# Kernel optimization log

Measured on AMD Instinct MI355X. Metric: run time of the kernel, lower is better.

The kernel has to match this reference:

```python
import jax, jax.numpy as jnp
import numpy as np

N, D_IN, D_OUT, E = 50000, 64, 64, 800000
NEG_SLOPE = 0.2  # PyG GATConv default leaky-relu slope


def setup_inputs() -> dict:
    key = jax.random.key(0)
    ks = jax.random.split(key, 11)
    s_in = 1.0 / np.sqrt(D_IN)
    s_out = 1.0 / np.sqrt(D_OUT)
    return {
        "x": jax.random.normal(ks[0], (N, D_IN), jnp.float32),
        "edge_index": jax.random.randint(ks[1], (2, E), 0, N, jnp.int32),
        "h": jax.random.normal(ks[2], (N, D_OUT), jnp.float32) * 0.1,
        "c": jax.random.normal(ks[3], (N, D_OUT), jnp.float32) * 0.1,
        "W": jax.random.normal(ks[4], (4, D_IN, D_OUT), jnp.float32) * s_in,
        "b": jax.random.normal(ks[5], (4, 1, D_OUT), jnp.float32) * 0.01,
        "Wsrc": jax.random.normal(ks[6], (4, D_OUT, D_OUT), jnp.float32) * s_out,
        "Wdst": jax.random.normal(ks[7], (4, D_OUT, D_OUT), jnp.float32) * s_out,
        "att_src": jax.random.normal(ks[8], (4, D_OUT), jnp.float32) * 0.1,
        "att_dst": jax.random.normal(ks[9], (4, D_OUT), jnp.float32) * 0.1,
        "gat_b": jax.random.normal(ks[10], (4, D_OUT), jnp.float32) * 0.01,
    }


def _gat(h, src, dst, Ws, Wd, a_s, a_d, bg, n):
    """GATConv(heads=1, add_self_loops=False) on edges src->dst."""
    hs = h @ Ws                      # [N, D] source-side projection
    hd = h @ Wd                      # [N, D] dest-side projection
    alpha_s = hs @ a_s               # [N]
    alpha_d = hd @ a_d               # [N]
    e = jax.nn.leaky_relu(alpha_s[src] + alpha_d[dst], NEG_SLOPE)  # [E]
    # numerically stable segment softmax over incoming edges per dst node
    m = jax.ops.segment_max(e, dst, num_segments=n)
    ex = jnp.exp(e - m[dst])
    denom = jax.ops.segment_sum(ex, dst, num_segments=n)
    w = ex / denom[dst]              # [E] attention weights
    out = jax.ops.segment_sum(w[:, None] * hs[src], dst, num_segments=n)
    return out + bg


def reference(x, edge_index, h, c, W, b, Wsrc, Wdst, att_src, att_dst, gat_b):
    src, dst = edge_index[0], edge_index[1]
    n = x.shape[0]

    def gate(g, act):
        pre = x @ W[g] + _gat(h, src, dst, Wsrc[g], Wdst[g],
                              att_src[g], att_dst[g], gat_b[g], n) + b[g]
        return act(pre)

    i = gate(0, jax.nn.sigmoid)
    f = gate(1, jax.nn.sigmoid)
    t = gate(2, jnp.tanh)
    c_new = f * c + i * t
    o = gate(3, jax.nn.sigmoid)   # output gate conv uses the OLD hidden state h
    h_new = o * jnp.tanh(c_new)
    return (h_new, c_new)
```

## Files before the change

### kernel.cpp

```cpp
#include <hip/hip_runtime.h>
#include <math.h>

#define NEG_SLOPE 0.2f

typedef float  f32x4 __attribute__((ext_vector_type(4)));
typedef short  s16x8 __attribute__((ext_vector_type(8)));

__device__ __forceinline__ unsigned short bfr(float a){
  unsigned u = __float_as_uint(a);
  return (unsigned short)((u + 0x7FFFu + ((u>>16)&1u)) >> 16);
}
__device__ __forceinline__ float bf2f(unsigned short s){
  return __uint_as_float(((unsigned)s)<<16);
}
__device__ __forceinline__ ushort4 packf4(float4 v){
  ushort4 r; r.x=bfr(v.x); r.y=bfr(v.y); r.z=bfr(v.z); r.w=bfr(v.w); return r;
}

__device__ __forceinline__ signed char q8(float v){
  int q = __float2int_rn(v * 128.f);
  q = q > 127 ? 127 : (q < -127 ? -127 : q);
  return (signed char)q;
}

__global__ void k_wvec_pack(const float* __restrict__ Wsrc, const float* __restrict__ Wdst,
                            const float* __restrict__ Wmain,
                            const float* __restrict__ att_src, const float* __restrict__ att_dst,
                            float* __restrict__ wvec, int* __restrict__ bcnt,
                            unsigned short* __restrict__ pw, unsigned short* __restrict__ ps){
  int tid = threadIdx.x;
  if (blockIdx.x == 0){
    if (tid < 128) bcnt[tid] = 0;
    int v = tid >> 6, t = tid & 63;
    const float* M = (v<4) ? (Wsrc + v*4096) : (Wdst + (v-4)*4096);
    const float* a = (v<4) ? (att_src + v*64) : (att_dst + (v-4)*64);
    float s = 0.f;
    for (int k=0;k<64;++k) s += M[t*64+k]*a[k];
    wvec[v*64+t] = s;
  } else {
    int vv = (blockIdx.x-1)*512 + tid;
    if (vv < 2048){
      int l = vv & 63, u = vv >> 6;
      int ct = u & 3, ks = (u>>2)&1, g = u>>3;
      int col = ct*16 + (l&15);
      int r0  = ks*32 + (l>>4)*8;
      #pragma unroll
      for (int j=0;j<8;++j){
        pw[vv*8+j] = bfr(Wmain[g*4096 + (r0+j)*64 + col]);
        ps[vv*8+j] = bfr(Wsrc [g*4096 + (r0+j)*64 + col]);
      }
    }
  }
}

__global__ __launch_bounds__(256) void k_pack(
    const float* __restrict__ x, const float* __restrict__ h,
    const float* __restrict__ wvec, const int* __restrict__ ei,
    unsigned short* __restrict__ xb, signed char* __restrict__ h8,
    float* __restrict__ alphas, int* __restrict__ bcnt, int shift, int N, int E){
  __shared__ float hl[32*65];
  __shared__ float wl[8*65];
  __shared__ int   cb[128];
  int tid = threadIdx.x;
  int nbase = blockIdx.x*32;
  int nlim = min(32, N-nbase);
  int cnt = nlim*16;
  if (tid < 128) cb[tid] = 0;
  {
    const float4* hsrc = (const float4*)(h + (size_t)nbase*64);
    const float4* xsrc = (const float4*)(x + (size_t)nbase*64);
    char4* hdst = (char4*)(h8 + (size_t)nbase*64);
    ushort4* xdst = (ushort4*)(xb + (size_t)nbase*64);
    for (int i=tid; i<cnt; i+=256){
      float4 v = hsrc[i];
      int n = i>>4, t4 = (i&15)*4;
      float* d = hl + n*65 + t4;
      d[0]=v.x; d[1]=v.y; d[2]=v.z; d[3]=v.w;
      hdst[i] = make_char4(q8(v.x), q8(v.y), q8(v.z), q8(v.w));
      xdst[i] = packf4(xsrc[i]);
    }
    for (int i=tid; i<512; i+=256) wl[(i>>6)*65 + (i&63)] = wvec[i];
  }
  __syncthreads();
  int v = tid & 7, n = tid >> 3;
  if (n < nlim){
    const float* hp = hl + n*65;
    const float* wp = wl + v*65;
    float s = 0.f;
    #pragma unroll
    for (int t=0;t<64;++t) s += hp[t]*wp[t];
    alphas[(size_t)(nbase+n)*8 + v] = s;
  }
  int Q = E >> 2;
  const int4* d4 = (const int4*)(ei + E);
  long gs = (long)gridDim.x*256;
  for (long q=(long)blockIdx.x*256+tid; q<Q; q+=gs){
    int4 d = d4[q];
    atomicAdd(&cb[d.x>>shift],1); atomicAdd(&cb[d.y>>shift],1);
    atomicAdd(&cb[d.z>>shift],1); atomicAdd(&cb[d.w>>shift],1);
  }
  int tail = E - (Q<<2);
  if (blockIdx.x == 0 && tid < tail) atomicAdd(&cb[ei[E+(Q<<2)+tid]>>shift],1);
  __syncthreads();
  if (tid < 128 && cb[tid]) atomicAdd(&bcnt[tid], cb[tid]);
}

__global__ void k_bscan(const int* __restrict__ bcnt, int* __restrict__ bbase,
                        int* __restrict__ bfill, int* __restrict__ rowptr,
                        int nbuck, int N, int E){
  __shared__ int s[128];
  int tid = threadIdx.x;
  int x = (tid<nbuck) ? bcnt[tid] : 0;
  s[tid] = x;
  __syncthreads();
  for (int off=1; off<128; off<<=1){
    int t = (tid>=off) ? s[tid-off] : 0;
    __syncthreads();
    s[tid] += t;
    __syncthreads();
  }
  if (tid<nbuck){ int e = s[tid]-x; bbase[tid]=e; bfill[tid]=e; }
  if (tid==0){ bbase[nbuck]=E; rowptr[N]=E; }
}

__global__ __launch_bounds__(256) void k_bin(
    const int* __restrict__ ei, int* __restrict__ bfill,
    int2* __restrict__ binned, int shift, int E){
  __shared__ int2 buf[2048];
  __shared__ int cnt[128], off[128], gbase[128];
  int tid = threadIdx.x;
  int c0 = blockIdx.x*2048;
  int m = min(2048, E - c0);
  if (m <= 0) return;
  for (int i=tid; i<128; i+=256) cnt[i] = 0;
  __syncthreads();
  int myb[8], myslot[8], mysrc[8], mydst[8];
  #pragma unroll
  for (int j=0;j<8;++j){
    int k = tid + j*256;
    if (k < m){
      int e = c0 + k;
      mysrc[j] = ei[e];
      mydst[j] = ei[E+e];
      int bkt = mydst[j] >> shift;
      myb[j] = bkt;
      myslot[j] = atomicAdd(&cnt[bkt], 1);
    } else myb[j] = -1;
  }
  __syncthreads();
  if (tid == 0){
    int acc = 0;
    for (int i=0;i<128;++i){ off[i] = acc; acc += cnt[i]; }
  }
  __syncthreads();
  #pragma unroll
  for (int j=0;j<8;++j)
    if (myb[j] >= 0) buf[off[myb[j]] + myslot[j]] = make_int2(mysrc[j], mydst[j]);
  if (tid < 128 && cnt[tid] > 0) gbase[tid] = atomicAdd(&bfill[tid], cnt[tid]);
  __syncthreads();
  for (int i=tid; i<m; i+=256){
    int2 p = buf[i];
    int bkt = p.y >> shift;
    binned[gbase[bkt] + (i - off[bkt])] = p;
  }
}

__global__ __launch_bounds__(1024) void k_place(
    const int2* __restrict__ binned, const int* __restrict__ bbase,
    int* __restrict__ rowptr, int* __restrict__ csr_src, int shift, int N){
  __shared__ int cnt[1024];
  __shared__ int tsum[1024];
  int tid = threadIdx.x;
  int d0 = blockIdx.x << shift;
  if (d0 >= N) return;
  int dpb = 1 << shift;
  int dlim = min(dpb, N - d0);
  if (tid < dpb) cnt[tid] = 0;
  __syncthreads();
  int base = bbase[blockIdx.x], end = bbase[blockIdx.x+1];
  for (int i = base + tid; i < end; i += 1024)
    atomicAdd(&cnt[binned[i].y - d0], 1);
  __syncthreads();
  int xv = (tid < dpb) ? cnt[tid] : 0;
  tsum[tid] = xv;
  __syncthreads();
  for (int off=1; off<1024; off<<=1){
    int t = (tid>=off) ? tsum[tid-off] : 0;
    __syncthreads();
    tsum[tid] += t;
    __syncthreads();
  }
  if (tid < dpb) cnt[tid] = tsum[tid] - xv + base;
  __syncthreads();
  if (tid < dlim) rowptr[d0+tid] = cnt[tid];
  __syncthreads();
  for (int i = base + tid; i < end; i += 1024){
    int2 p = binned[i];
    int pos = atomicAdd(&cnt[p.y - d0], 1);
    csr_src[pos] = p.x;
  }
}

__global__ __launch_bounds__(256) void k_agg(
    const int* __restrict__ csr_src, const int* __restrict__ rowptr,
    const float* __restrict__ alphas,
    const signed char* __restrict__ h8, unsigned short* __restrict__ aggb, int N){
  __shared__ float4 wb4[4][64];
  __shared__ int    sb[4][64];
  int wave = threadIdx.x>>6, lane = threadIdx.x&63;
  int dst = blockIdx.x*4 + wave;
  if (dst >= N) return;
  int base = rowptr[dst];
  int d = rowptr[dst+1] - base;
  float4 ad = ((const float4*)alphas)[(size_t)dst*2+1];
  float ss0=0.f,ss1=0.f,ss2=0.f,ss3=0.f;
  float a0=0.f,a1=0.f,a2=0.f,a3=0.f;
  for (int c0=0; c0<d; c0+=64){
    int cnt = min(64, d-c0);
    if (lane < cnt){
      int s = csr_src[base+c0+lane];
      float4 as = ((const float4*)alphas)[(size_t)s*2];
      float e0=as.x+ad.x; e0 = e0>0.f ? e0 : NEG_SLOPE*e0; float x0=__expf(e0); ss0+=x0;
      float e1=as.y+ad.y; e1 = e1>0.f ? e1 : NEG_SLOPE*e1; float x1=__expf(e1); ss1+=x1;
      float e2=as.z+ad.z; e2 = e2>0.f ? e2 : NEG_SLOPE*e2; float x2=__expf(e2); ss2+=x2;
      float e3=as.w+ad.w; e3 = e3>0.f ? e3 : NEG_SLOPE*e3; float x3=__expf(e3); ss3+=x3;
      sb[wave][lane] = s;
      wb4[wave][lane] = make_float4(x0,x1,x2,x3);
    }
    asm volatile("" ::: "memory");
    int j = 0;
    for (; j+3 < cnt; j += 4){
      int s0_ = sb[wave][j],   s1_ = sb[wave][j+1];
      int s2_ = sb[wave][j+2], s3_ = sb[wave][j+3];
      float4 w0_ = wb4[wave][j],   w1_ = wb4[wave][j+1];
      float4 w2_ = wb4[wave][j+2], w3_ = wb4[wave][j+3];
      float h0_ = (float)h8[(size_t)s0_*64 + lane];
      float h1_ = (float)h8[(size_t)s1_*64 + lane];
      float h2_ = (float)h8[(size_t)s2_*64 + lane];
      float h3_ = (float)h8[(size_t)s3_*64 + lane];
      a0 += w0_.x*h0_; a1 += w0_.y*h0_; a2 += w0_.z*h0_; a3 += w0_.w*h0_;
      a0 += w1_.x*h1_; a1 += w1_.y*h1_; a2 += w1_.z*h1_; a3 += w1_.w*h1_;
      a0 += w2_.x*h2_; a1 += w2_.y*h2_; a2 += w2_.z*h2_; a3 += w2_.w*h2_;
      a0 += w3_.x*h3_; a1 += w3_.y*h3_; a2 += w3_.z*h3_; a3 += w3_.w*h3_;
    }
    for (; j < cnt; ++j){
      int sj = sb[wave][j];
      float4 wj = wb4[wave][j];
      float hv = (float)h8[(size_t)sj*64 + lane];
      a0 += wj.x*hv; a1 += wj.y*hv; a2 += wj.z*hv; a3 += wj.w*hv;
    }
    asm volatile("" ::: "memory");
  }
  #pragma unroll
  for (int off=32; off; off>>=1){
    ss0 += __shfl_xor(ss0, off, 64);
    ss1 += __shfl_xor(ss1, off, 64);
    ss2 += __shfl_xor(ss2, off, 64);
    ss3 += __shfl_xor(ss3, off, 64);
  }
  size_t o = (size_t)dst*64 + lane;
  size_t NE = (size_t)N*64;
  if (d>0){
    aggb[o]      = bfr(a0/(ss0*128.f));
    aggb[NE+o]   = bfr(a1/(ss1*128.f));
    aggb[2*NE+o] = bfr(a2/(ss2*128.f));
    aggb[3*NE+o] = bfr(a3/(ss3*128.f));
  } else {
    aggb[o] = 0; aggb[NE+o] = 0; aggb[2*NE+o] = 0; aggb[3*NE+o] = 0;
  }
}

__global__ __launch_bounds__(256) void k_fused(
    const unsigned short* __restrict__ xb, const unsigned short* __restrict__ aggb,
    const unsigned short* __restrict__ pw, const unsigned short* __restrict__ ps,
    const float* __restrict__ b, const float* __restrict__ gat_b,
    const float* __restrict__ c, float* __restrict__ out, int N){
  __shared__ unsigned short Pl[4][32][68];
  int tid = threadIdx.x, g = tid>>6, l = tid&63;
  int lr = l & 15;
  int lq = l >> 4;
  int nbase = blockIdx.x*32;
  int nlim = min(32, N-nbase);

  s16x8 BW[2][4], BS[2][4];
  #pragma unroll
  for (int ks=0; ks<2; ++ks){
    #pragma unroll
    for (int ct=0; ct<4; ++ct){
      size_t idx = ((size_t)((g*2+ks)*4+ct)*64 + l)*8;
      BW[ks][ct] = *(const s16x8*)(pw + idx);
      BS[ks][ct] = *(const s16x8*)(ps + idx);
    }
  }

  s16x8 AX[2][2], AG[2][2];
  #pragma unroll
  for (int rt=0; rt<2; ++rt){
    int row = nbase + rt*16 + lr;
    if (row >= N) row = N-1;
    #pragma unroll
    for (int ks=0; ks<2; ++ks){
      AX[rt][ks] = *(const s16x8*)(xb   + (size_t)row*64 + ks*32 + lq*8);
      AG[rt][ks] = *(const s16x8*)(aggb + ((size_t)g*N + row)*64 + ks*32 + lq*8);
    }
  }

  #pragma unroll
  for (int rt=0; rt<2; ++rt){
    #pragma unroll
    for (int ct=0; ct<4; ++ct){
      int col = ct*16 + lr;
      float bias = b[g*64 + col] + gat_b[g*64 + col];
      f32x4 acc = {bias, bias, bias, bias};
      #pragma unroll
      for (int ks=0; ks<2; ++ks){
        acc = __builtin_amdgcn_mfma_f32_16x16x32_bf16(AX[rt][ks], BW[ks][ct], acc, 0,0,0);
        acc = __builtin_amdgcn_mfma_f32_16x16x32_bf16(AG[rt][ks], BS[ks][ct], acc, 0,0,0);
      }
      #pragma unroll
      for (int r=0;r<4;++r)
        Pl[g][rt*16 + lq*4 + r][col] = bfr(acc[r]);
    }
  }
  __syncthreads();

  size_t NE = (size_t)N*64;
  #pragma unroll
  for (int n=0; n<8; ++n){
    int node = g*8 + n;
    if (node < nlim){
      size_t o = (size_t)(nbase + node)*64 + l;
      float p0 = bf2f(Pl[0][node][l]);
      float p1 = bf2f(Pl[1][node][l]);
      float p2 = bf2f(Pl[2][node][l]);
      float p3 = bf2f(Pl[3][node][l]);
      float ig = 1.f/(1.f + __expf(-p0));
      float fg = 1.f/(1.f + __expf(-p1));
      float tg = tanhf(p2);
      float og = 1.f/(1.f + __expf(-p3));
      float cn = fg*c[o] + ig*tg;
      out[o]      = og*tanhf(cn);
      out[NE + o] = cn;
    }
  }
}

extern "C" void kernel_launch(void* const* d_in, const int* in_sizes, int n_in,
                              void* d_out, int out_size, void* d_ws, size_t ws_size,
                              hipStream_t stream){
  const float* x       = (const float*)d_in[0];
  const int*   ei      = (const int*)d_in[1];
  const float* h       = (const float*)d_in[2];
  const float* c       = (const float*)d_in[3];
  const float* W       = (const float*)d_in[4];
  const float* b       = (const float*)d_in[5];
  const float* Wsrc    = (const float*)d_in[6];
  const float* Wdst    = (const float*)d_in[7];
  const float* att_src = (const float*)d_in[8];
  const float* att_dst = (const float*)d_in[9];
  const float* gat_b   = (const float*)d_in[10];
  float* out = (float*)d_out;

  int N = in_sizes[0] / 64;
  int E = in_sizes[1] / 2;

  int shift = 9;
  while (((N + (1<<shift) - 1) >> shift) > 128) shift++;
  int nbuck = (N + (1<<shift) - 1) >> shift;

  unsigned short* aggb = (unsigned short*)d_ws;
  unsigned short* xb   = aggb + (size_t)4*N*64;
  signed char*    h8   = (signed char*)(xb + (size_t)N*64);
  unsigned short* pw   = (unsigned short*)(h8 + (size_t)N*64);
  unsigned short* ps   = pw   + 16384;
  float* alphas = (float*)(ps + 16384);
  int* csr_src  = (int*)(alphas + (size_t)N*8);
  int2* binned  = (int2*)(csr_src + ((E+3)&~3));
  int* rowptr   = (int*)(binned + E);
  int* bcnt     = rowptr + N + 1;
  int* bbase    = bcnt + 128;
  int* bfill    = bbase + 129;
  float* wvec   = (float*)(bfill + 128);

  k_wvec_pack<<<9, 512, 0, stream>>>(Wsrc, Wdst, W, att_src, att_dst, wvec, bcnt, pw, ps);
  k_pack  <<<(N+31)/32, 256, 0, stream>>>(x, h, wvec, ei, xb, h8, alphas, bcnt, shift, N, E);
  k_bscan <<<1, 128, 0, stream>>>(bcnt, bbase, bfill, rowptr, nbuck, N, E);
  k_bin   <<<(E + 2047)/2048, 256, 0, stream>>>(ei, bfill, binned, shift, E);
  k_place <<<nbuck, 1024, 0, stream>>>(binned, bbase, rowptr, csr_src, shift, N);
  k_agg   <<<(N+3)/4, 256, 0, stream>>>(csr_src, rowptr, alphas, h8, aggb, N);
  k_fused <<<(N+31)/32, 256, 0, stream>>>(xb, aggb, pw, ps, b, gat_b, c, out, N);
}
```

Baseline: 127.9 us.

## Precompute bf16 source attention scores during binning and store in CSR order

Source-side attention logits are gathered in the binning kernel, rounded to bf16, and carried through the binned records into a new CSR-ordered weight array. The aggregation kernel then reads these scores contiguously instead of gathering 16-byte alpha rows per edge by source index. The cost is wider binned records, an extra per-edge array write and read, a random gather moved into k_bin, and reduced precision of alpha_s.

```diff
diff --git a/kernel.cpp b/kernel.cpp
--- a/kernel.cpp
+++ b/kernel.cpp
@@ -124,9 +124,9 @@
 }
 
 __global__ __launch_bounds__(256) void k_bin(
-    const int* __restrict__ ei, int* __restrict__ bfill,
-    int2* __restrict__ binned, int shift, int E){
-  __shared__ int2 buf[2048];
+    const int* __restrict__ ei, const float* __restrict__ alphas,
+    int* __restrict__ bfill, int4* __restrict__ binned, int shift, int E){
+  __shared__ int4 buf[2048];
   __shared__ int cnt[128], off[128], gbase[128];
   int tid = threadIdx.x;
   int c0 = blockIdx.x*2048;
@@ -135,13 +135,18 @@
   for (int i=tid; i<128; i+=256) cnt[i] = 0;
   __syncthreads();
   int myb[8], myslot[8], mysrc[8], mydst[8];
+  int myw0[8], myw1[8];
   #pragma unroll
   for (int j=0;j<8;++j){
     int k = tid + j*256;
     if (k < m){
       int e = c0 + k;
-      mysrc[j] = ei[e];
+      int s = ei[e];
+      mysrc[j] = s;
       mydst[j] = ei[E+e];
+      float4 as = ((const float4*)alphas)[(size_t)s*2];
+      myw0[j] = (int)(((unsigned)bfr(as.x)) | (((unsigned)bfr(as.y))<<16));
+      myw1[j] = (int)(((unsigned)bfr(as.z)) | (((unsigned)bfr(as.w))<<16));
       int bkt = mydst[j] >> shift;
       myb[j] = bkt;
       myslot[j] = atomicAdd(&cnt[bkt], 1);
@@ -155,19 +160,20 @@
   __syncthreads();
   #pragma unroll
   for (int j=0;j<8;++j)
-    if (myb[j] >= 0) buf[off[myb[j]] + myslot[j]] = make_int2(mysrc[j], mydst[j]);
+    if (myb[j] >= 0) buf[off[myb[j]] + myslot[j]] = make_int4(mysrc[j], mydst[j], myw0[j], myw1[j]);
   if (tid < 128 && cnt[tid] > 0) gbase[tid] = atomicAdd(&bfill[tid], cnt[tid]);
   __syncthreads();
   for (int i=tid; i<m; i+=256){
-    int2 p = buf[i];
+    int4 p = buf[i];
     int bkt = p.y >> shift;
     binned[gbase[bkt] + (i - off[bkt])] = p;
   }
 }
 
 __global__ __launch_bounds__(1024) void k_place(
-    const int2* __restrict__ binned, const int* __restrict__ bbase,
-    int* __restrict__ rowptr, int* __restrict__ csr_src, int shift, int N){
+    const int4* __restrict__ binned, const int* __restrict__ bbase,
+    int* __restrict__ rowptr, int* __restrict__ csr_src, int2* __restrict__ csr_w,
+    int shift, int N){
   __shared__ int cnt[1024];
   __shared__ int tsum[1024];
   int tid = threadIdx.x;
@@ -195,15 +201,16 @@
   if (tid < dlim) rowptr[d0+tid] = cnt[tid];
   __syncthreads();
   for (int i = base + tid; i < end; i += 1024){
-    int2 p = binned[i];
+    int4 p = binned[i];
     int pos = atomicAdd(&cnt[p.y - d0], 1);
     csr_src[pos] = p.x;
+    csr_w[pos] = make_int2(p.z, p.w);
   }
 }
 
 __global__ __launch_bounds__(256) void k_agg(
-    const int* __restrict__ csr_src, const int* __restrict__ rowptr,
-    const float* __restrict__ alphas,
+    const int* __restrict__ csr_src, const int2* __restrict__ csr_w,
+    const int* __restrict__ rowptr, const float* __restrict__ alphas,
     const signed char* __restrict__ h8, unsigned short* __restrict__ aggb, int N){
   __shared__ float4 wb4[4][64];
   __shared__ int    sb[4][64];
@@ -219,11 +226,11 @@
     int cnt = min(64, d-c0);
     if (lane < cnt){
       int s = csr_src[base+c0+lane];
-      float4 as = ((const float4*)alphas)[(size_t)s*2];
-      float e0=as.x+ad.x; e0 = e0>0.f ? e0 : NEG_SLOPE*e0; float x0=__expf(e0); ss0+=x0;
-      float e1=as.y+ad.y; e1 = e1>0.f ? e1 : NEG_SLOPE*e1; float x1=__expf(e1); ss1+=x1;
-      float e2=as.z+ad.z; e2 = e2>0.f ? e2 : NEG_SLOPE*e2; float x2=__expf(e2); ss2+=x2;
-      float e3=as.w+ad.w; e3 = e3>0.f ? e3 : NEG_SLOPE*e3; float x3=__expf(e3); ss3+=x3;
+      int2 wp = csr_w[base+c0+lane];
+      float e0 = bf2f((unsigned short)(wp.x & 0xFFFF)) + ad.x; e0 = e0>0.f ? e0 : NEG_SLOPE*e0; float x0=__expf(e0); ss0+=x0;
+      float e1 = bf2f((unsigned short)((unsigned)wp.x >> 16)) + ad.y; e1 = e1>0.f ? e1 : NEG_SLOPE*e1; float x1=__expf(e1); ss1+=x1;
+      float e2 = bf2f((unsigned short)(wp.y & 0xFFFF)) + ad.z; e2 = e2>0.f ? e2 : NEG_SLOPE*e2; float x2=__expf(e2); ss2+=x2;
+      float e3 = bf2f((unsigned short)((unsigned)wp.y >> 16)) + ad.w; e3 = e3>0.f ? e3 : NEG_SLOPE*e3; float x3=__expf(e3); ss3+=x3;
       sb[wave][lane] = s;
       wb4[wave][lane] = make_float4(x0,x1,x2,x3);
     }
@@ -375,8 +382,9 @@
   unsigned short* ps   = pw   + 16384;
   float* alphas = (float*)(ps + 16384);
   int* csr_src  = (int*)(alphas + (size_t)N*8);
-  int2* binned  = (int2*)(csr_src + ((E+3)&~3));
-  int* rowptr   = (int*)(binned + E);
+  int4* binned  = (int4*)(csr_src + ((E+3)&~3));
+  int2* csr_w   = (int2*)(binned + E);
+  int* rowptr   = (int*)(csr_w + E);
   int* bcnt     = rowptr + N + 1;
   int* bbase    = bcnt + 128;
   int* bfill    = bbase + 129;
@@ -385,8 +393,8 @@
   k_wvec_pack<<<9, 512, 0, stream>>>(Wsrc, Wdst, W, att_src, att_dst, wvec, bcnt, pw, ps);
   k_pack  <<<(N+31)/32, 256, 0, stream>>>(x, h, wvec, ei, xb, h8, alphas, bcnt, shift, N, E);
   k_bscan <<<1, 128, 0, stream>>>(bcnt, bbase, bfill, rowptr, nbuck, N, E);
-  k_bin   <<<(E + 2047)/2048, 256, 0, stream>>>(ei, bfill, binned, shift, E);
-  k_place <<<nbuck, 1024, 0, stream>>>(binned, bbase, rowptr, csr_src, shift, N);
-  k_agg   <<<(N+3)/4, 256, 0, stream>>>(csr_src, rowptr, alphas, h8, aggb, N);
+  k_bin   <<<(E + 2047)/2048, 256, 0, stream>>>(ei, alphas, bfill, binned, shift, E);
+  k_place <<<nbuck, 1024, 0, stream>>>(binned, bbase, rowptr, csr_src, csr_w, shift, N);
+  k_agg   <<<(N+3)/4, 256, 0, stream>>>(csr_src, csr_w, rowptr, alphas, h8, aggb, N);
   k_fused <<<(N+31)/32, 256, 0, stream>>>(xb, aggb, pw, ps, b, gat_b, c, out, N);
 }
```

After: 139.0 us. 8.7% more time.
